# Optimization experiments

Hardware: AMD Instinct MI355X
Metric: run time of the kernel (lower is better)

## Reference

```python
import jax, jax.numpy as jnp
import numpy as np

N = 50000        # nodes
E = 800000       # edges (before self-loops)
IN_DIM = 128
HID = 32         # per-head hidden channels, conv1
OUT = 32         # per-head output channels, conv2
H = 4            # attention heads
NEG_SLOPE = 0.2  # PyG GATConv default


def setup_inputs() -> dict:
    key = jax.random.key(0)
    ks = jax.random.split(key, 12)
    x = jax.random.normal(ks[0], (N, IN_DIM), dtype=jnp.float32)
    edge_index = jax.random.randint(ks[1], (2, E), 0, N, dtype=jnp.int32)
    s = 0.05
    W1 = jax.random.normal(ks[2], (IN_DIM, H * HID), dtype=jnp.float32) * s
    a_src1 = jax.random.normal(ks[3], (H, HID), dtype=jnp.float32) * s
    a_dst1 = jax.random.normal(ks[4], (H, HID), dtype=jnp.float32) * s
    b1 = jnp.zeros((H * HID,), dtype=jnp.float32)
    W2 = jax.random.normal(ks[5], (H * HID, H * OUT), dtype=jnp.float32) * s
    a_src2 = jax.random.normal(ks[6], (H, OUT), dtype=jnp.float32) * s
    a_dst2 = jax.random.normal(ks[7], (H, OUT), dtype=jnp.float32) * s
    b2 = jnp.zeros((H * OUT,), dtype=jnp.float32)
    return {"x": x, "edge_index": edge_index,
            "W1": W1, "a_src1": a_src1, "a_dst1": a_dst1, "b1": b1,
            "W2": W2, "a_src2": a_src2, "a_dst2": a_dst2, "b2": b2}


def _gat_conv(x, src, dst, W, a_src, a_dst, b, heads, ch):
    # linear transform: [N, heads, ch]
    h = (x @ W).reshape(-1, heads, ch)
    # per-node attention logits [N, heads]
    al_src = jnp.einsum('nhc,hc->nh', h, a_src)
    al_dst = jnp.einsum('nhc,hc->nh', h, a_dst)
    # per-edge logits, leaky relu  [Etot, heads]
    e = jax.nn.leaky_relu(al_src[src] + al_dst[dst], negative_slope=NEG_SLOPE)
    # softmax over incoming edges of each destination node
    m = jax.lax.stop_gradient(jax.ops.segment_max(e, dst, num_segments=N))
    ex = jnp.exp(e - m[dst])
    denom = jax.ops.segment_sum(ex, dst, num_segments=N)
    alpha = ex / denom[dst]                      # [Etot, heads]
    # weighted scatter-aggregate of source features
    out = jax.ops.segment_sum(alpha[:, :, None] * h[src], dst, num_segments=N)
    return out.reshape(N, heads * ch) + b


def reference(x, edge_index, W1, a_src1, a_dst1, b1, W2, a_src2, a_dst2, b2):
    # PyG GATConv add_self_loops=True
    loops = jnp.arange(N, dtype=edge_index.dtype)
    src = jnp.concatenate([edge_index[0], loops])
    dst = jnp.concatenate([edge_index[1], loops])
    # eval mode: dropout is identity
    h = _gat_conv(x, src, dst, W1, a_src1, a_dst1, b1, H, HID)
    h = jax.nn.elu(h)
    out = _gat_conv(h, src, dst, W2, a_src2, a_dst2, b2, H, OUT)
    return out
```

## Files before the change

kernel.cpp:

```cpp
#include <hip/hip_runtime.h>
#include <hip/hip_bf16.h>

#define NN 50000
#define EE 800000
#define ETOT (EE + NN)
#define F 128
#define HEADS 4
#define MT 64
#define NB ((NN + 1023) / 1024)

__device__ __forceinline__ unsigned short f32_to_bf16(float f) {
    unsigned int u = __float_as_uint(f);
    u += 0x7fffu + ((u >> 16) & 1u);
    return (unsigned short)(u >> 16);
}
__device__ __forceinline__ float bflo(unsigned int u) { return __uint_as_float(u << 16); }
__device__ __forceinline__ float bfhi(unsigned int u) { return __uint_as_float(u & 0xffff0000u); }


__launch_bounds__(256)
__global__ void gemm_count(const float* __restrict__ A, const float* __restrict__ W,
                           const float* __restrict__ a_src, const float* __restrict__ a_dst,
                           unsigned short* __restrict__ Cb, float* __restrict__ als,
                           float* __restrict__ ald, int M,
                           const int* __restrict__ ei, int* __restrict__ counts,
                           int gemm_blocks) {
    __shared__ float xs[MT][F];
    if ((int)blockIdx.x >= gemm_blocks) {
        int e = (blockIdx.x - gemm_blocks) * 256 + threadIdx.x;
        if (e < ETOT) {
            int dst = (e < EE) ? ei[EE + e] : (e - EE);
            atomicAdd(&counts[dst], 1);
        }
        return;
    }
    int tid = threadIdx.x;
    int row0 = blockIdx.x * MT;

    for (int i = tid; i < MT * F / 4; i += 256) {
        int r  = i >> 5;
        int c4 = i & 31;
        int gr = row0 + r;
        float4 v = (gr < M) ? ((const float4*)A)[(size_t)gr * 32 + c4]
                            : make_float4(0.f, 0.f, 0.f, 0.f);
        ((float4*)&xs[r][0])[c4] = v;
    }
    __syncthreads();

    int cg = (tid & 31) * 4;
    int rg = (tid >> 5) * 8;
    float acc[8][4];
#pragma unroll
    for (int r = 0; r < 8; r++)
#pragma unroll
        for (int j = 0; j < 4; j++) acc[r][j] = 0.f;

#pragma unroll 4
    for (int k = 0; k < F; k += 4) {
        float4 w0 = *(const float4*)&W[(k + 0) * F + cg];
        float4 w1 = *(const float4*)&W[(k + 1) * F + cg];
        float4 w2 = *(const float4*)&W[(k + 2) * F + cg];
        float4 w3 = *(const float4*)&W[(k + 3) * F + cg];
#pragma unroll
        for (int r = 0; r < 8; r++) {
            float4 xv = *(const float4*)&xs[rg + r][k];
            acc[r][0] += xv.x * w0.x + xv.y * w1.x + xv.z * w2.x + xv.w * w3.x;
            acc[r][1] += xv.x * w0.y + xv.y * w1.y + xv.z * w2.y + xv.w * w3.y;
            acc[r][2] += xv.x * w0.z + xv.y * w1.z + xv.z * w2.z + xv.w * w3.z;
            acc[r][3] += xv.x * w0.w + xv.y * w1.w + xv.z * w2.w + xv.w * w3.w;
        }
    }

    int lane = tid & 63;
    int head = (tid & 31) >> 3;
    float4 asv = *(const float4*)&a_src[head * 32 + (lane & 7) * 4];
    float4 adv = *(const float4*)&a_dst[head * 32 + (lane & 7) * 4];
#pragma unroll
    for (int r = 0; r < 8; r++) {
        int gr = row0 + rg + r;
        if (gr < M) {
            ushort4 bv;
            bv.x = f32_to_bf16(acc[r][0]);
            bv.y = f32_to_bf16(acc[r][1]);
            bv.z = f32_to_bf16(acc[r][2]);
            bv.w = f32_to_bf16(acc[r][3]);
            *(ushort4*)&Cb[(size_t)gr * F + cg] = bv;
        }
        float ps = acc[r][0] * asv.x + acc[r][1] * asv.y + acc[r][2] * asv.z + acc[r][3] * asv.w;
        float pd = acc[r][0] * adv.x + acc[r][1] * adv.y + acc[r][2] * adv.z + acc[r][3] * adv.w;
        ps += __shfl_xor(ps, 1); ps += __shfl_xor(ps, 2); ps += __shfl_xor(ps, 4);
        pd += __shfl_xor(pd, 1); pd += __shfl_xor(pd, 2); pd += __shfl_xor(pd, 4);
        if ((lane & 7) == 0 && gr < M) {
            als[gr * HEADS + head] = ps;
            ald[gr * HEADS + head] = pd;
        }
    }
}


__launch_bounds__(1024)
__global__ void scan_block_k(const int* __restrict__ counts, int* __restrict__ row_ptr,
                             int* __restrict__ bsum, int n) {
    int tid = threadIdx.x;
    int i = blockIdx.x * 1024 + tid;
    int v = (i < n) ? counts[i] : 0;
    int lane = tid & 63;
    int wave = tid >> 6;
    int x = v;
#pragma unroll
    for (int off = 1; off < 64; off <<= 1) {
        int t = __shfl_up(x, off, 64);
        if (lane >= off) x += t;
    }
    __shared__ int wsum[16];
    if (lane == 63) wsum[wave] = x;
    __syncthreads();
    if (wave == 0) {
        int w = (lane < 16) ? wsum[lane] : 0;
#pragma unroll
        for (int off = 1; off < 16; off <<= 1) {
            int t = __shfl_up(w, off, 64);
            if (lane >= off) w += t;
        }
        if (lane < 16) wsum[lane] = w;
    }
    __syncthreads();
    int base = (wave > 0) ? wsum[wave - 1] : 0;
    int incl = base + x;
    if (i < n) row_ptr[i] = incl - v;
    if (tid == 1023) bsum[blockIdx.x] = incl;
}

__launch_bounds__(256)
__global__ void scan_add_k(int* __restrict__ row_ptr, const int* __restrict__ bsum, int n) {
    __shared__ int off_s[NB];
    if (threadIdx.x < 64) {
        int lane = threadIdx.x;
        int v = (lane < NB) ? bsum[lane] : 0;
        int x = v;
#pragma unroll
        for (int o = 1; o < 64; o <<= 1) {
            int t = __shfl_up(x, o, 64);
            if (lane >= o) x += t;
        }
        if (lane < NB) off_s[lane] = x - v;
    }
    __syncthreads();
    int i = blockIdx.x * blockDim.x + threadIdx.x;
    if (i < n) row_ptr[i] += off_s[i >> 10];
    if (i == 0) row_ptr[n] = ETOT;
}

__global__ void fill_k(const int* __restrict__ ei, const int* __restrict__ row_ptr,
                       int* __restrict__ counts, int* __restrict__ csr_src) {
    int e = blockIdx.x * blockDim.x + threadIdx.x;
    if (e >= ETOT) return;
    int src, dst;
    if (e < EE) { src = ei[e]; dst = ei[EE + e]; }
    else        { src = e - EE; dst = e - EE; }
    int c = atomicSub(&counts[dst], 1);
    csr_src[row_ptr[dst] + c - 1] = src;
}


__launch_bounds__(256)
__global__ void aggregate(const unsigned short* __restrict__ hb, const float* __restrict__ als,
                          const float* __restrict__ ald, const int* __restrict__ row_ptr,
                          const int* __restrict__ csr_src, const float* __restrict__ bias,
                          float* __restrict__ out, int apply_elu) {
    int wave = threadIdx.x >> 6;
    int n = blockIdx.x * 4 + wave;
    if (n >= NN) return;
    int lane = threadIdx.x & 63;
    int g  = lane >> 4;
    int cl = lane & 15;
    int head = cl >> 2;
    float aldv = ald[n * HEADS + head];
    int jb = row_ptr[n], je = row_ptr[n + 1];

    float acc[8];
#pragma unroll
    for (int i = 0; i < 8; i++) acc[i] = 0.f;
    float den = 0.f;

    int j = jb + g;
    for (; j + 4 < je; j += 8) {
        int s0 = csr_src[j];
        int s1 = csr_src[j + 4];
        float e0 = als[s0 * HEADS + head] + aldv;
        float e1 = als[s1 * HEADS + head] + aldv;
        uint4 r0 = *(const uint4*)&hb[(size_t)s0 * F + cl * 8];
        uint4 r1 = *(const uint4*)&hb[(size_t)s1 * F + cl * 8];
        e0 = (e0 > 0.f) ? e0 : 0.2f * e0;
        e1 = (e1 > 0.f) ? e1 : 0.2f * e1;
        float p0 = __expf(e0);
        float p1 = __expf(e1);
        den += p0 + p1;
        acc[0] += p0 * bflo(r0.x); acc[1] += p0 * bfhi(r0.x);
        acc[2] += p0 * bflo(r0.y); acc[3] += p0 * bfhi(r0.y);
        acc[4] += p0 * bflo(r0.z); acc[5] += p0 * bfhi(r0.z);
        acc[6] += p0 * bflo(r0.w); acc[7] += p0 * bfhi(r0.w);
        acc[0] += p1 * bflo(r1.x); acc[1] += p1 * bfhi(r1.x);
        acc[2] += p1 * bflo(r1.y); acc[3] += p1 * bfhi(r1.y);
        acc[4] += p1 * bflo(r1.z); acc[5] += p1 * bfhi(r1.z);
        acc[6] += p1 * bflo(r1.w); acc[7] += p1 * bfhi(r1.w);
    }
    if (j < je) {
        int s = csr_src[j];
        float e = als[s * HEADS + head] + aldv;
        uint4 raw = *(const uint4*)&hb[(size_t)s * F + cl * 8];
        e = (e > 0.f) ? e : 0.2f * e;
        float p = __expf(e);
        den += p;
        acc[0] += p * bflo(raw.x); acc[1] += p * bfhi(raw.x);
        acc[2] += p * bflo(raw.y); acc[3] += p * bfhi(raw.y);
        acc[4] += p * bflo(raw.z); acc[5] += p * bfhi(raw.z);
        acc[6] += p * bflo(raw.w); acc[7] += p * bfhi(raw.w);
    }

#pragma unroll
    for (int i = 0; i < 8; i++) {
        acc[i] += __shfl_xor(acc[i], 16);
        acc[i] += __shfl_xor(acc[i], 32);
    }
    den += __shfl_xor(den, 16);
    den += __shfl_xor(den, 32);

    if (g == 0) {
        float inv = 1.f / den;
        float v[8];
#pragma unroll
        for (int i = 0; i < 8; i++) {
            v[i] = acc[i] * inv + bias[cl * 8 + i];
            if (apply_elu) v[i] = (v[i] > 0.f) ? v[i] : (__expf(v[i]) - 1.f);
        }
        float4* op = (float4*)&out[(size_t)n * F + cl * 8];
        op[0] = make_float4(v[0], v[1], v[2], v[3]);
        op[1] = make_float4(v[4], v[5], v[6], v[7]);
    }
}


extern "C" void kernel_launch(void* const* d_in, const int* in_sizes, int n_in,
                              void* d_out, int out_size, void* d_ws, size_t ws_size,
                              hipStream_t stream) {
    const float* x   = (const float*)d_in[0];
    const int*   ei  = (const int*)d_in[1];
    const float* W1  = (const float*)d_in[2];
    const float* as1 = (const float*)d_in[3];
    const float* ad1 = (const float*)d_in[4];
    const float* b1  = (const float*)d_in[5];
    const float* W2  = (const float*)d_in[6];
    const float* as2 = (const float*)d_in[7];
    const float* ad2 = (const float*)d_in[8];
    const float* b2  = (const float*)d_in[9];
    float* out = (float*)d_out;

    char* ws = (char*)d_ws;
    size_t off = 0;
    auto alloc = [&](size_t bytes) {
        void* p = ws + off;
        off += (bytes + 255) & ~(size_t)255;
        return p;
    };
    unsigned short* hb = (unsigned short*)alloc((size_t)NN * F * 2);
    float* als     = (float*)alloc((size_t)NN * HEADS * 4);
    float* ald     = (float*)alloc((size_t)NN * HEADS * 4);
    int*   counts  = (int*)alloc((size_t)NN * 4);
    int*   row_ptr = (int*)alloc((size_t)(NN + 1) * 4);
    int*   bsum    = (int*)alloc((size_t)NB * 4);
    int*   csr_src = (int*)alloc((size_t)ETOT * 4);

    int GG = (NN + MT - 1) / MT;
    int CG = (ETOT + 255) / 256;
    int agg_grid = (NN + 3) / 4;

    (void)hipMemsetAsync(counts, 0, (size_t)NN * 4, stream);

    gemm_count<<<GG + CG, 256, 0, stream>>>(x, W1, as1, ad1, hb, als, ald, NN,
                                            ei, counts, GG);
    scan_block_k<<<NB, 1024, 0, stream>>>(counts, row_ptr, bsum, NN);
    scan_add_k<<<(NN + 255) / 256, 256, 0, stream>>>(row_ptr, bsum, NN);
    fill_k<<<CG, 256, 0, stream>>>(ei, row_ptr, counts, csr_src);
    aggregate<<<agg_grid, 256, 0, stream>>>(hb, als, ald, row_ptr, csr_src, b1, out, 1);

    gemm_count<<<GG, 256, 0, stream>>>(out, W2, as2, ad2, hb, als, ald, NN,
                                       (const int*)nullptr, (int*)nullptr, GG);
    aggregate<<<agg_grid, 256, 0, stream>>>(hb, als, ald, row_ptr, csr_src, b2, out, 0);
}
```

Measured before the change: 317.9 us.

## Use split-bf16 MFMA for the node linear transforms

Replaces the fp32 FMA GEMM with bf16 MFMA 16x16x32 instructions. Both operands are split into high and low bf16 parts, and three products are summed to approximate fp32 precision. A small pre-pass kernel packs W1 and W2 into the MFMA fragment layout. Results are staged through LDS for the bf16 output store and the attention-logit dot products. This adds an extra kernel launch and per-element conversion work, and loses a little precision relative to full fp32.

Result: no change. 314.0 us (-1.2%).

```diff
diff --git a/kernel.cpp b/kernel.cpp
--- a/kernel.cpp
+++ b/kernel.cpp
@@ -9,23 +9,57 @@
 #define MT 64
 #define NB ((NN + 1023) / 1024)
 
+typedef __bf16 bf16x8 __attribute__((ext_vector_type(8)));
+typedef float  f32x4  __attribute__((ext_vector_type(4)));
+
 __device__ __forceinline__ unsigned short f32_to_bf16(float f) {
     unsigned int u = __float_as_uint(f);
     u += 0x7fffu + ((u >> 16) & 1u);
     return (unsigned short)(u >> 16);
 }
+__device__ __forceinline__ float bf16bits_to_f32(unsigned short s) {
+    return __uint_as_float(((unsigned int)s) << 16);
+}
 __device__ __forceinline__ float bflo(unsigned int u) { return __uint_as_float(u << 16); }
 __device__ __forceinline__ float bfhi(unsigned int u) { return __uint_as_float(u & 0xffff0000u); }
 
+union BU { unsigned short u[8]; bf16x8 v; };
+
+
+__global__ void wpack_k(const float* __restrict__ W1, const float* __restrict__ W2,
+                        unsigned short* __restrict__ wf) {
+    int t = blockIdx.x * blockDim.x + threadIdx.x;
+    if (t >= 2 * 2048) return;
+    int which = t >> 11;
+    int rem = t & 2047;
+    int lane = rem & 63;
+    int tile = rem >> 6;
+    int kt = tile >> 3, nt = tile & 7;
+    int q = lane >> 4, c = lane & 15;
+    const float* W = which ? W2 : W1;
+    BU vh, vl;
+#pragma unroll
+    for (int j = 0; j < 8; j++) {
+        float w = W[(kt * 32 + q * 8 + j) * F + nt * 16 + c];
+        unsigned short hb = f32_to_bf16(w);
+        vh.u[j] = hb;
+        vl.u[j] = f32_to_bf16(w - bf16bits_to_f32(hb));
+    }
+    size_t base_h = ((size_t)(which * 2 + 0) * 2048 + tile * 64 + lane) * 8;
+    size_t base_l = ((size_t)(which * 2 + 1) * 2048 + tile * 64 + lane) * 8;
+    *(bf16x8*)&wf[base_h] = vh.v;
+    *(bf16x8*)&wf[base_l] = vl.v;
+}
+
 
 __launch_bounds__(256)
-__global__ void gemm_count(const float* __restrict__ A, const float* __restrict__ W,
-                           const float* __restrict__ a_src, const float* __restrict__ a_dst,
-                           unsigned short* __restrict__ Cb, float* __restrict__ als,
-                           float* __restrict__ ald, int M,
-                           const int* __restrict__ ei, int* __restrict__ counts,
-                           int gemm_blocks) {
-    __shared__ float xs[MT][F];
+__global__ void gemm_mfma(const float* __restrict__ A, const unsigned short* __restrict__ wf,
+                          const float* __restrict__ a_src, const float* __restrict__ a_dst,
+                          unsigned short* __restrict__ Cb, float* __restrict__ als,
+                          float* __restrict__ ald, int M,
+                          const int* __restrict__ ei, int* __restrict__ counts,
+                          int gemm_blocks) {
+    __shared__ float lds[4][16 * 132];
     if ((int)blockIdx.x >= gemm_blocks) {
         int e = (blockIdx.x - gemm_blocks) * 256 + threadIdx.x;
         if (e < ETOT) {
@@ -35,65 +69,77 @@
         return;
     }
     int tid = threadIdx.x;
-    int row0 = blockIdx.x * MT;
-
-    for (int i = tid; i < MT * F / 4; i += 256) {
-        int r  = i >> 5;
-        int c4 = i & 31;
-        int gr = row0 + r;
-        float4 v = (gr < M) ? ((const float4*)A)[(size_t)gr * 32 + c4]
-                            : make_float4(0.f, 0.f, 0.f, 0.f);
-        ((float4*)&xs[r][0])[c4] = v;
-    }
+    int w = tid >> 6, lane = tid & 63;
+    int m = lane & 15, q = lane >> 4;
+    int row0 = blockIdx.x * MT + w * 16;
+
+    int ar = row0 + m; if (ar >= M) ar = 0;
+    const float* arow = A + (size_t)ar * F + q * 8;
+    const unsigned short* wfh = wf;
+    const unsigned short* wfl = wf + 2048 * 8;
+
+    f32x4 acc[8];
+#pragma unroll
+    for (int nt = 0; nt < 8; nt++) acc[nt] = (f32x4){0.f, 0.f, 0.f, 0.f};
+
+#pragma unroll
+    for (int kt = 0; kt < 4; kt++) {
+        float4 a0 = *(const float4*)(arow + kt * 32);
+        float4 a1 = *(const float4*)(arow + kt * 32 + 4);
+        float av[8] = {a0.x, a0.y, a0.z, a0.w, a1.x, a1.y, a1.z, a1.w};
+        BU ah, al;
+#pragma unroll
+        for (int j = 0; j < 8; j++) {
+            unsigned short hb = f32_to_bf16(av[j]);
+            ah.u[j] = hb;
+            al.u[j] = f32_to_bf16(av[j] - bf16bits_to_f32(hb));
+        }
+#pragma unroll
+        for (int nt = 0; nt < 8; nt++) {
+            size_t bo = ((size_t)(kt * 8 + nt) * 64 + lane) * 8;
+            bf16x8 bh = *(const bf16x8*)&wfh[bo];
+            bf16x8 bl = *(const bf16x8*)&wfl[bo];
+            acc[nt] = __builtin_amdgcn_mfma_f32_16x16x32_bf16(ah.v, bh, acc[nt], 0, 0, 0);
+            acc[nt] = __builtin_amdgcn_mfma_f32_16x16x32_bf16(al.v, bh, acc[nt], 0, 0, 0);
+            acc[nt] = __builtin_amdgcn_mfma_f32_16x16x32_bf16(ah.v, bl, acc[nt], 0, 0, 0);
+        }
+    }
+
+    float* L = lds[w];
+#pragma unroll
+    for (int nt = 0; nt < 8; nt++)
+#pragma unroll
+        for (int r = 0; r < 4; r++)
+            L[(q * 4 + r) * 132 + nt * 16 + m] = acc[nt][r];
     __syncthreads();
 
-    int cg = (tid & 31) * 4;
-    int rg = (tid >> 5) * 8;
-    float acc[8][4];
-#pragma unroll
-    for (int r = 0; r < 8; r++)
-#pragma unroll
-        for (int j = 0; j < 4; j++) acc[r][j] = 0.f;
-
-#pragma unroll 4
-    for (int k = 0; k < F; k += 4) {
-        float4 w0 = *(const float4*)&W[(k + 0) * F + cg];
-        float4 w1 = *(const float4*)&W[(k + 1) * F + cg];
-        float4 w2 = *(const float4*)&W[(k + 2) * F + cg];
-        float4 w3 = *(const float4*)&W[(k + 3) * F + cg];
-#pragma unroll
-        for (int r = 0; r < 8; r++) {
-            float4 xv = *(const float4*)&xs[rg + r][k];
-            acc[r][0] += xv.x * w0.x + xv.y * w1.x + xv.z * w2.x + xv.w * w3.x;
-            acc[r][1] += xv.x * w0.y + xv.y * w1.y + xv.z * w2.y + xv.w * w3.y;
-            acc[r][2] += xv.x * w0.z + xv.y * w1.z + xv.z * w2.z + xv.w * w3.z;
-            acc[r][3] += xv.x * w0.w + xv.y * w1.w + xv.z * w2.w + xv.w * w3.w;
-        }
-    }
-
-    int lane = tid & 63;
-    int head = (tid & 31) >> 3;
-    float4 asv = *(const float4*)&a_src[head * 32 + (lane & 7) * 4];
-    float4 adv = *(const float4*)&a_dst[head * 32 + (lane & 7) * 4];
-#pragma unroll
-    for (int r = 0; r < 8; r++) {
-        int gr = row0 + rg + r;
-        if (gr < M) {
-            ushort4 bv;
-            bv.x = f32_to_bf16(acc[r][0]);
-            bv.y = f32_to_bf16(acc[r][1]);
-            bv.z = f32_to_bf16(acc[r][2]);
-            bv.w = f32_to_bf16(acc[r][3]);
-            *(ushort4*)&Cb[(size_t)gr * F + cg] = bv;
-        }
-        float ps = acc[r][0] * asv.x + acc[r][1] * asv.y + acc[r][2] * asv.z + acc[r][3] * asv.w;
-        float pd = acc[r][0] * adv.x + acc[r][1] * adv.y + acc[r][2] * adv.z + acc[r][3] * adv.w;
-        ps += __shfl_xor(ps, 1); ps += __shfl_xor(ps, 2); ps += __shfl_xor(ps, 4);
-        pd += __shfl_xor(pd, 1); pd += __shfl_xor(pd, 2); pd += __shfl_xor(pd, 4);
-        if ((lane & 7) == 0 && gr < M) {
-            als[gr * HEADS + head] = ps;
-            ald[gr * HEADS + head] = pd;
-        }
+    int rr = lane >> 2;
+    int head = lane & 3;
+    int c0 = head * 32;
+    int gr = row0 + rr;
+    float v[32];
+#pragma unroll
+    for (int i = 0; i < 8; i++)
+        *(float4*)&v[i * 4] = *(const float4*)&L[rr * 132 + c0 + i * 4];
+
+    if (gr < M) {
+#pragma unroll
+        for (int i = 0; i < 4; i++) {
+            uint4 pk;
+            pk.x = (unsigned)f32_to_bf16(v[i * 8 + 0]) | ((unsigned)f32_to_bf16(v[i * 8 + 1]) << 16);
+            pk.y = (unsigned)f32_to_bf16(v[i * 8 + 2]) | ((unsigned)f32_to_bf16(v[i * 8 + 3]) << 16);
+            pk.z = (unsigned)f32_to_bf16(v[i * 8 + 4]) | ((unsigned)f32_to_bf16(v[i * 8 + 5]) << 16);
+            pk.w = (unsigned)f32_to_bf16(v[i * 8 + 6]) | ((unsigned)f32_to_bf16(v[i * 8 + 7]) << 16);
+            *(uint4*)&Cb[(size_t)gr * F + c0 + i * 8] = pk;
+        }
+        float ps = 0.f, pd = 0.f;
+#pragma unroll
+        for (int i = 0; i < 32; i++) {
+            ps += v[i] * a_src[c0 + i];
+            pd += v[i] * a_dst[c0 + i];
+        }
+        als[gr * HEADS + head] = ps;
+        ald[gr * HEADS + head] = pd;
     }
 }
 
@@ -270,21 +316,23 @@
     int*   row_ptr = (int*)alloc((size_t)(NN + 1) * 4);
     int*   bsum    = (int*)alloc((size_t)NB * 4);
     int*   csr_src = (int*)alloc((size_t)ETOT * 4);
+    unsigned short* wf = (unsigned short*)alloc((size_t)4 * 2048 * 8 * 2);
 
     int GG = (NN + MT - 1) / MT;
     int CG = (ETOT + 255) / 256;
     int agg_grid = (NN + 3) / 4;
 
     (void)hipMemsetAsync(counts, 0, (size_t)NN * 4, stream);
-
-    gemm_count<<<GG + CG, 256, 0, stream>>>(x, W1, as1, ad1, hb, als, ald, NN,
-                                            ei, counts, GG);
+    wpack_k<<<16, 256, 0, stream>>>(W1, W2, wf);
+
+    gemm_mfma<<<GG + CG, 256, 0, stream>>>(x, wf, as1, ad1, hb, als, ald, NN,
+                                           ei, counts, GG);
     scan_block_k<<<NB, 1024, 0, stream>>>(counts, row_ptr, bsum, NN);
     scan_add_k<<<(NN + 255) / 256, 256, 0, stream>>>(row_ptr, bsum, NN);
     fill_k<<<CG, 256, 0, stream>>>(ei, row_ptr, counts, csr_src);
     aggregate<<<agg_grid, 256, 0, stream>>>(hb, als, ald, row_ptr, csr_src, b1, out, 1);
 
-    gemm_count<<<GG, 256, 0, stream>>>(out, W2, as2, ad2, hb, als, ald, NN,
-                                       (const int*)nullptr, (int*)nullptr, GG);
+    gemm_mfma<<<GG, 256, 0, stream>>>(out, wf + (size_t)2 * 2048 * 8, as2, ad2, hb, als, ald, NN,
+                                      (const int*)nullptr, (int*)nullptr, GG);
     aggregate<<<agg_grid, 256, 0, stream>>>(hb, als, ald, row_ptr, csr_src, b2, out, 0);
 }
```
